# Optimization experiments

Measured on AMD Instinct MI355X. Metric: run time of the kernel, lower is better.

Reference implementation:

```python
import jax, jax.numpy as jnp
from jax import lax
import numpy as np

STATE_DIM = 64
CHANNELS = 128
SEQ_LEN = 4096
BATCH = 16
DT_MIN, DT_MAX = 1e-3, 1e-1


def hippo(n):
    # HiPPO-LegS construction, matching the torch staticmethod
    ar = jnp.arange(n, dtype=jnp.float32)
    P = jnp.sqrt(1.0 + 2.0 * ar)
    A = P[:, None] * P[None, :]
    A = jnp.tril(A) - jnp.diag(ar)
    B = jnp.sqrt(2.0 * ar + 1.0)
    return -A, B[:, None]


def setup_inputs() -> dict:
    key = jax.random.key(0)
    k_u, k_c = jax.random.split(key)
    A, B = hippo(STATE_DIM)
    # xavier_normal_ for C: std = sqrt(2/(fan_in+fan_out))
    std = float(np.sqrt(2.0 / (CHANNELS + STATE_DIM)))
    C = jax.random.normal(k_c, (CHANNELS, STATE_DIM), dtype=jnp.float32) * std
    D = jnp.ones((CHANNELS, 1), dtype=jnp.float32)
    # deterministic dt at log-midpoint of [dt_min, dt_max]
    dt = jnp.exp(jnp.array([(np.log(DT_MIN) + np.log(DT_MAX)) / 2.0], dtype=jnp.float32))
    u = jax.random.normal(k_u, (BATCH, SEQ_LEN), dtype=jnp.float32)
    return {"u": u, "A": A, "B": B, "C": C, "D": D, "dt": dt}


def reference(u, A, B, C, D, dt):
    # Training-path forward of LinearStateSpaceLayer (conv-kernel construction + conv1d)
    b, L = u.shape
    n = A.shape[0]
    dt_s = dt[0]
    I = jnp.eye(n, dtype=A.dtype)
    BL = jnp.linalg.inv(I - 0.5 * dt_s * A)            # bilinear discretization
    A_bar = BL @ (I + 0.5 * dt_s * A)                  # (n, n)
    B_bar = (BL * dt_s) @ B                            # (n, 1)

    # kernel k[j] = C @ A_bar^j @ B_bar for j = 0..L-1, via a scan of matvecs
    def step(v, _):
        return A_bar @ v, v
    _, vs = lax.scan(step, B_bar[:, 0], None, length=L)  # (L, n), vs[j] = A_bar^j B_bar
    k_causal = vs @ C.T                                  # (L, channels)
    # torch ordering: k_conv[c, 0, i] = C A_bar^{L-1-i} B_bar = k_causal[L-1-i, c]
    k_conv = k_causal[::-1].T[:, None, :]                # (channels, 1, L)

    # torch F.conv1d is cross-correlation; lax conv_general_dilated matches
    y = lax.conv_general_dilated(
        u[:, None, :], k_conv,
        window_strides=(1,), padding=[(L - 1, L - 1)],
        dimension_numbers=("NCH", "OIH", "NCH"),
    )[:, :, :L]                                          # (b, channels, L)

    # skip term: (u.unsqueeze(-1) @ D.T).transpose(-1,-2) == u[b,t] * D[c,0]
    y = y + u[:, None, :] * D[None, :, :]                # (b, channels, L)
    return y
```

## Files before the change

### kernel.cpp

```cpp
#include <hip/hip_runtime.h>

#define NS   64
#define CH   128
#define LSEQ 4096
#define NB   16
#define SCH  64
#define MCH  64
#define ST   68
#define CP   128

#define WS_ABAR 0
#define WS_A16  4096
#define WS_VS   8192
#define WS_BBAR 12288

#define X0_IDX(b, m) (((size_t)(b) * CH) * LSEQ + (size_t)(m) * SCH)

#define P_VSS  0
#define P_XCW  1024
#define P_XBS  1280
#define P_PLE  1536
#define P_PART 1792
#define P_A16  2048

#define FMA44(av, bv)                                                          \
    a0.x += av.x * bv.x; a0.y += av.x * bv.y; a0.z += av.x * bv.z; a0.w += av.x * bv.w; \
    a1.x += av.y * bv.x; a1.y += av.y * bv.y; a1.z += av.y * bv.z; a1.w += av.y * bv.w; \
    a2.x += av.z * bv.x; a2.y += av.z * bv.y; a2.z += av.z * bv.z; a2.w += av.z * bv.w; \
    a3.x += av.w * bv.x; a3.y += av.w * bv.y; a3.z += av.w * bv.z; a3.w += av.w * bv.w;


template<bool WT>
__device__ __forceinline__ void mm_square(const float* __restrict__ cm,
                                          const float* __restrict__ cmt,
                                          float* __restrict__ nm,
                                          float* __restrict__ nmt, int e) {
    const int l = e & 63;
    const int si0 = 16 * ((e >> 6) & 3) + 4 * (l >> 4);
    const int sj0 = 4 * (l & 15);
    const int kmax = si0 + 4;
    float4 a0 = {0,0,0,0}, a1 = {0,0,0,0}, a2 = {0,0,0,0}, a3 = {0,0,0,0};
    for (int k = 0; k < kmax; k += 4) {
        float4 av0 = *(const float4*)&cmt[(k + 0) * ST + si0];
        float4 bv0 = *(const float4*)&cm [(k + 0) * ST + sj0];
        float4 av1 = *(const float4*)&cmt[(k + 1) * ST + si0];
        float4 bv1 = *(const float4*)&cm [(k + 1) * ST + sj0];
        float4 av2 = *(const float4*)&cmt[(k + 2) * ST + si0];
        float4 bv2 = *(const float4*)&cm [(k + 2) * ST + sj0];
        float4 av3 = *(const float4*)&cmt[(k + 3) * ST + si0];
        float4 bv3 = *(const float4*)&cm [(k + 3) * ST + sj0];
        FMA44(av0, bv0)
        FMA44(av1, bv1)
        FMA44(av2, bv2)
        FMA44(av3, bv3)
    }
    *(float4*)&nm[(si0 + 0) * ST + sj0] = a0;
    *(float4*)&nm[(si0 + 1) * ST + sj0] = a1;
    *(float4*)&nm[(si0 + 2) * ST + sj0] = a2;
    *(float4*)&nm[(si0 + 3) * ST + sj0] = a3;
    if (WT) {
        float4 t0 = {a0.x, a1.x, a2.x, a3.x};
        float4 t1 = {a0.y, a1.y, a2.y, a3.y};
        float4 t2 = {a0.z, a1.z, a2.z, a3.z};
        float4 t3 = {a0.w, a1.w, a2.w, a3.w};
        *(float4*)&nmt[(sj0 + 0) * ST + si0] = t0;
        *(float4*)&nmt[(sj0 + 1) * ST + si0] = t1;
        *(float4*)&nmt[(sj0 + 2) * ST + si0] = t2;
        *(float4*)&nmt[(sj0 + 3) * ST + si0] = t3;
    }
}

__device__ __forceinline__ void mm_sq42(const float* __restrict__ cm,
                                        const float* __restrict__ cmt,
                                        float* __restrict__ nm,
                                        float* __restrict__ nmt, int tid) {
    const int si0 = 4 * (tid >> 5);
    const int sj0 = 2 * (tid & 31);
    const int kmax = si0 + 4;
    float2 a0 = {0,0}, a1 = {0,0}, a2 = {0,0}, a3 = {0,0};
#pragma unroll 4
    for (int k = 0; k < kmax; ++k) {
        float4 av = *(const float4*)&cmt[k * ST + si0];
        float2 bv = *(const float2*)&cm [k * ST + sj0];
        a0.x += av.x * bv.x; a0.y += av.x * bv.y;
        a1.x += av.y * bv.x; a1.y += av.y * bv.y;
        a2.x += av.z * bv.x; a2.y += av.z * bv.y;
        a3.x += av.w * bv.x; a3.y += av.w * bv.y;
    }
    *(float2*)&nm[(si0 + 0) * ST + sj0] = a0;
    *(float2*)&nm[(si0 + 1) * ST + sj0] = a1;
    *(float2*)&nm[(si0 + 2) * ST + sj0] = a2;
    *(float2*)&nm[(si0 + 3) * ST + sj0] = a3;
    float4 t0 = {a0.x, a1.x, a2.x, a3.x};
    float4 t1 = {a0.y, a1.y, a2.y, a3.y};
    *(float4*)&nmt[(sj0 + 0) * ST + si0] = t0;
    *(float4*)&nmt[(sj0 + 1) * ST + si0] = t1;
}

__device__ __forceinline__ void vs_expand1(const float* __restrict__ cmt,
                                           float* __restrict__ VT,
                                           int iq, int j, int mexp) {
    const int i0 = 4 * iq;
    float4 acc = {0,0,0,0};
#pragma unroll 8
    for (int k = 0; k < NS; ++k) {
        float4 av = *(const float4*)&cmt[k * ST + i0];
        float bk = VT[k * ST + j];
        acc.x += av.x * bk; acc.y += av.y * bk;
        acc.z += av.z * bk; acc.w += av.w * bk;
    }
    VT[(i0 + 0) * ST + mexp + j] = acc.x;
    VT[(i0 + 1) * ST + mexp + j] = acc.y;
    VT[(i0 + 2) * ST + mexp + j] = acc.z;
    VT[(i0 + 3) * ST + mexp + j] = acc.w;
}

__device__ __forceinline__ void pq_step(const float* __restrict__ Acol,
                                        const float* __restrict__ xle,
                                        float* __restrict__ outb, int r0, int e) {
    const int g = e >> 4, i0 = 4 * (e & 15);
    const float* bp = &xle[(4 * g + r0) * NS];
    float4 acc = *(const float4*)&xle[(4 * g + r0 + 1) * NS + i0];
#pragma unroll 8
    for (int k = 0; k < NS; ++k) {
        float4 av = *(const float4*)&Acol[k * ST + i0];
        float bk = bp[k];
        acc.x = fmaf(av.x, bk, acc.x); acc.y = fmaf(av.y, bk, acc.y);
        acc.z = fmaf(av.z, bk, acc.z); acc.w = fmaf(av.w, bk, acc.w);
    }
    *(float4*)&outb[g * ST + i0] = acc;
}

__device__ __forceinline__ void y_step512(const float* __restrict__ A128col,
                                          const float* __restrict__ P,
                                          const float* __restrict__ Q,
                                          float* __restrict__ Y, int e) {
    const int g = e >> 5, c0 = 2 * (e & 31);
    const float* bp = &P[g * ST];
    float2 acc = *(const float2*)&Q[g * ST + c0];
#pragma unroll 8
    for (int k = 0; k < NS; ++k) {
        float2 av = *(const float2*)&A128col[k * ST + c0];
        float bk = bp[k];
        acc.x = fmaf(av.x, bk, acc.x); acc.y = fmaf(av.y, bk, acc.y);
    }
    *(float2*)&Y[g * ST + c0] = acc;
}

__device__ __forceinline__ void inner_step(const float* __restrict__ Acol,
                                           const float* __restrict__ xle,
                                           float* __restrict__ stash, int r, int e) {
    const int g = e >> 4, i0 = 4 * (e & 15);
    const int mp = 4 * g + r - 1;
    float4 acc = *(const float4*)&xle[mp * NS + i0];
    const float* xp = &stash[mp * ST];
#pragma unroll 8
    for (int k = 0; k < NS; ++k) {
        float4 av = *(const float4*)&Acol[k * ST + i0];
        float xk = xp[k];
        acc.x = fmaf(av.x, xk, acc.x); acc.y = fmaf(av.y, xk, acc.y);
        acc.z = fmaf(av.z, xk, acc.z); acc.w = fmaf(av.w, xk, acc.w);
    }
    *(float4*)&stash[(mp + 1) * ST + i0] = acc;
}

__device__ __forceinline__ void inner512(const float* __restrict__ Acol,
                                         const float* __restrict__ xle,
                                         float* __restrict__ stash, int r, int e) {
    const int g = e >> 5, c0 = 2 * (e & 31);
    const int mp = 4 * g + r - 1;
    float2 acc = *(const float2*)&xle[mp * NS + c0];
    const float* xp = &stash[mp * ST];
#pragma unroll 8
    for (int k = 0; k < NS; ++k) {
        float2 av = *(const float2*)&Acol[k * ST + c0];
        float xk = xp[k];
        acc.x = fmaf(av.x, xk, acc.x); acc.y = fmaf(av.y, xk, acc.y);
    }
    *(float2*)&stash[(mp + 1) * ST + c0] = acc;
}

__device__ __forceinline__ void e1u_step(const float* __restrict__ A128col,
                                         const float* __restrict__ P,
                                         float* __restrict__ stash, int e) {
    const int g = e >> 4, i0 = 4 * (e & 15);
    const float* xp = &stash[(4 * g) * ST];
    float4 acc = *(const float4*)&P[g * ST + i0];
#pragma unroll 8
    for (int k = 0; k < NS; ++k) {
        float4 av = *(const float4*)&A128col[k * ST + i0];
        float xk = xp[k];
        acc.x = fmaf(av.x, xk, acc.x); acc.y = fmaf(av.y, xk, acc.y);
        acc.z = fmaf(av.z, xk, acc.z); acc.w = fmaf(av.w, xk, acc.w);
    }
    *(float4*)&stash[(4 * g + 2) * ST + i0] = acc;
}

__global__ __launch_bounds__(512) void k_sb(const float* __restrict__ u,
                                            const float* __restrict__ A,
                                            const float* __restrict__ Bv,
                                            const float* __restrict__ dtp,
                                            float* __restrict__ ws,
                                            float* __restrict__ out) {
    __shared__ __align__(16) float Mrow[NS * ST];
    __shared__ __align__(16) float Mcol[(NS + 1) * ST];
    __shared__ __align__(16) float Nrow[NS * ST];
    __shared__ __align__(16) float Ncol[NS * ST];
    __shared__ __align__(16) float VT[NS * ST];
    __shared__ __align__(16) float uT[NS * ST];
    __shared__ __align__(16) float vsS[NS * NS];
    __shared__ __align__(16) float xleS[MCH * NS];
    __shared__ __align__(16) float bcol[NS];
    __shared__ float rdiag[NS], xcS[NS];
    float* const stash = uT;
    float* const HbP = vsS;
    float* const HbQ = vsS + 16 * ST;
    float* const HbY = vsS + 32 * ST;
    const int tid = threadIdx.x;
    const int b = blockIdx.x;
    const float dt = dtp[0];
    const float hdt = 0.5f * dt;

    for (int o = tid; o < NS * NS; o += 512) {
        int i = o >> 6, k = o & 63;
        float a = A[o];
        float d = (i == k) ? 1.0f : 0.0f;
        Nrow[i * ST + k] = d - hdt * a;
        Ncol[k * ST + i] = d + hdt * a;
    }
    if (tid < NS) {
        bcol[tid]  = dt * Bv[tid];
        rdiag[tid] = 1.0f / (1.0f - hdt * A[tid * NS + tid]);
    }
    __syncthreads();

    {
        const int jj = tid & 63;
#pragma unroll
        for (int rep = 0; rep < 2; ++rep) {
            const int m0 = 4 * (tid >> 6) + 32 * rep;
            float4 v;
            v.x = u[b * LSEQ + (m0 + 0) * SCH + 63 - jj];
            v.y = u[b * LSEQ + (m0 + 1) * SCH + 63 - jj];
            v.z = u[b * LSEQ + (m0 + 2) * SCH + 63 - jj];
            v.w = u[b * LSEQ + (m0 + 3) * SCH + 63 - jj];
            *(float4*)&uT[jj * ST + m0] = v;
        }
    }

    if (tid <= NS) {
        float xr[NS];
        const float* t2b = (tid < NS) ? &Ncol[tid * ST] : bcol;
#pragma unroll
        for (int I = 0; I < 16; ++I) {
            const int i0 = 4 * I;
            float4 t2 = *(const float4*)&t2b[i0];
            float a0 = t2.x, a1 = t2.y, a2 = t2.z, a3 = t2.w;
#pragma unroll
            for (int k = 0; k < i0; k += 4) {
                float4 n0 = *(const float4*)&Nrow[(i0 + 0) * ST + k];
                float4 n1 = *(const float4*)&Nrow[(i0 + 1) * ST + k];
                float4 n2 = *(const float4*)&Nrow[(i0 + 2) * ST + k];
                float4 n3 = *(const float4*)&Nrow[(i0 + 3) * ST + k];
                a0 -= n0.x * xr[k] + n0.y * xr[k + 1] + n0.z * xr[k + 2] + n0.w * xr[k + 3];
                a1 -= n1.x * xr[k] + n1.y * xr[k + 1] + n1.z * xr[k + 2] + n1.w * xr[k + 3];
                a2 -= n2.x * xr[k] + n2.y * xr[k + 1] + n2.z * xr[k + 2] + n2.w * xr[k + 3];
                a3 -= n3.x * xr[k] + n3.y * xr[k + 1] + n3.z * xr[k + 2] + n3.w * xr[k + 3];
            }
            float4 rd  = *(const float4*)&rdiag[i0];
            float4 nb1 = *(const float4*)&Nrow[(i0 + 1) * ST + i0];
            float4 nb2 = *(const float4*)&Nrow[(i0 + 2) * ST + i0];
            float4 nb3 = *(const float4*)&Nrow[(i0 + 3) * ST + i0];
            float x0 = a0 * rd.x;
            float x1 = (a1 - nb1.x * x0) * rd.y;
            float x2 = (a2 - nb2.x * x0 - nb2.y * x1) * rd.z;
            float x3 = (a3 - nb3.x * x0 - nb3.y * x1 - nb3.z * x2) * rd.w;
            xr[i0 + 0] = x0; xr[i0 + 1] = x1; xr[i0 + 2] = x2; xr[i0 + 3] = x3;
        }
        float* xrow = &Mcol[tid * ST];
#pragma unroll
        for (int k = 0; k < NS; k += 4) {
            float4 v = {xr[k], xr[k + 1], xr[k + 2], xr[k + 3]};
            *(float4*)&xrow[k] = v;
        }
    }
    __syncthreads();

    if (tid < 256) {
        const int i0 = 4 * (tid >> 4), j0 = 4 * (tid & 15);
        float4 r0 = *(const float4*)&Mcol[(j0 + 0) * ST + i0];
        float4 r1 = *(const float4*)&Mcol[(j0 + 1) * ST + i0];
        float4 r2 = *(const float4*)&Mcol[(j0 + 2) * ST + i0];
        float4 r3 = *(const float4*)&Mcol[(j0 + 3) * ST + i0];
        float4 w0 = {r0.x, r1.x, r2.x, r3.x};
        float4 w1 = {r0.y, r1.y, r2.y, r3.y};
        float4 w2 = {r0.z, r1.z, r2.z, r3.z};
        float4 w3 = {r0.w, r1.w, r2.w, r3.w};
        *(float4*)&Mrow[(i0 + 0) * ST + j0] = w0;
        *(float4*)&Mrow[(i0 + 1) * ST + j0] = w1;
        *(float4*)&Mrow[(i0 + 2) * ST + j0] = w2;
        *(float4*)&Mrow[(i0 + 3) * ST + j0] = w3;
        if (b == 0) {
            *(float4*)&ws[WS_ABAR + (i0 + 0) * NS + j0] = w0;
            *(float4*)&ws[WS_ABAR + (i0 + 1) * NS + j0] = w1;
            *(float4*)&ws[WS_ABAR + (i0 + 2) * NS + j0] = w2;
            *(float4*)&ws[WS_ABAR + (i0 + 3) * NS + j0] = w3;
        }
    }
    if (b == 1 && tid < 16)
        *(float4*)&ws[WS_BBAR + 4 * tid] = *(const float4*)&Mcol[NS * ST + 4 * tid];
    if (tid < NS) VT[tid * ST + 0] = Mcol[NS * ST + tid];
    __syncthreads();

    float *cm = Mrow, *cmt = Mcol, *nm = Nrow, *nmt = Ncol;
    for (int s = 1; s <= 6; ++s) {
        if (s <= 4) {
            mm_sq42(cm, cmt, nm, nmt, tid);
            const int mexp = 1 << (s - 1);
            if (tid < 16 * mexp) {
                vs_expand1(cmt, VT, tid & 15, tid >> 4, mexp);
            }
        } else if (tid < 256) {
            mm_square<true>(cm, cmt, nm, nmt, tid);
        } else {
            const int e = tid - 256;
            const int iq = e & 15;
            if (s == 5) {
                vs_expand1(cmt, VT, iq, e >> 4, 16);
            } else {
                const int j0 = 2 * (e >> 4);
                const int i0 = 4 * iq;
                float4 c0 = {0,0,0,0}, c1 = {0,0,0,0};
#pragma unroll 8
                for (int k = 0; k < NS; ++k) {
                    float4 av = *(const float4*)&cmt[k * ST + i0];
                    float2 bv = *(const float2*)&VT[k * ST + j0];
                    c0.x += av.x * bv.x; c0.y += av.y * bv.x;
                    c0.z += av.z * bv.x; c0.w += av.w * bv.x;
                    c1.x += av.x * bv.y; c1.y += av.y * bv.y;
                    c1.z += av.z * bv.y; c1.w += av.w * bv.y;
                }
                float2 w0 = {c0.x, c1.x}, w1 = {c0.y, c1.y};
                float2 w2 = {c0.z, c1.z}, w3 = {c0.w, c1.w};
                *(float2*)&VT[(i0 + 0) * ST + 32 + j0] = w0;
                *(float2*)&VT[(i0 + 1) * ST + 32 + j0] = w1;
                *(float2*)&VT[(i0 + 2) * ST + 32 + j0] = w2;
                *(float2*)&VT[(i0 + 3) * ST + 32 + j0] = w3;
            }
        }
        __syncthreads();
        { float* t = cm; cm = nm; nm = t; t = cmt; cmt = nmt; nmt = t; }
        if (s == 4 && b == 2) {
            for (int o = tid; o < (NS * NS) / 4; o += 512) {
                int r = o >> 4, c4 = (o & 15) * 4;
                *(float4*)&ws[WS_A16 + r * NS + c4] = *(const float4*)&cm[r * ST + c4];
            }
        }
    }

    if (tid < 256) {
        const int i0 = 4 * (tid >> 4), j0 = 4 * (tid & 15);
        float4 v0 = *(const float4*)&VT[(i0 + 0) * ST + j0];
        float4 v1 = *(const float4*)&VT[(i0 + 1) * ST + j0];
        float4 v2 = *(const float4*)&VT[(i0 + 2) * ST + j0];
        float4 v3 = *(const float4*)&VT[(i0 + 3) * ST + j0];
        float4 w0 = {v0.x, v1.x, v2.x, v3.x};
        float4 w1 = {v0.y, v1.y, v2.y, v3.y};
        float4 w2 = {v0.z, v1.z, v2.z, v3.z};
        float4 w3 = {v0.w, v1.w, v2.w, v3.w};
        *(float4*)&vsS[(j0 + 0) * NS + i0] = w0;
        *(float4*)&vsS[(j0 + 1) * NS + i0] = w1;
        *(float4*)&vsS[(j0 + 2) * NS + i0] = w2;
        *(float4*)&vsS[(j0 + 3) * NS + i0] = w3;
        if (b == 3) {
            *(float4*)&ws[WS_VS + (j0 + 0) * NS + i0] = w0;
            *(float4*)&ws[WS_VS + (j0 + 1) * NS + i0] = w1;
            *(float4*)&ws[WS_VS + (j0 + 2) * NS + i0] = w2;
            *(float4*)&ws[WS_VS + (j0 + 3) * NS + i0] = w3;
        }
    } else {
        mm_square<true>(Mrow, Mcol, Nrow, Ncol, tid - 256);
    }
    __syncthreads();

    if (tid < 256) {
        const int ig = tid & 15, mg = tid >> 4;
        float4 a0 = {0,0,0,0}, a1 = {0,0,0,0}, a2 = {0,0,0,0}, a3 = {0,0,0,0};
#pragma unroll 4
        for (int j = 0; j < NS; j += 2) {
            float4 am  = *(const float4*)&uT[j * ST + 4 * mg];
            float4 bi  = *(const float4*)&vsS[j * NS + 4 * ig];
            float4 am2 = *(const float4*)&uT[(j + 1) * ST + 4 * mg];
            float4 bi2 = *(const float4*)&vsS[(j + 1) * NS + 4 * ig];
            FMA44(am, bi)
            FMA44(am2, bi2)
        }
        *(float4*)&xleS[(4 * mg + 0) * NS + 4 * ig] = a0;
        *(float4*)&xleS[(4 * mg + 1) * NS + 4 * ig] = a1;
        *(float4*)&xleS[(4 * mg + 2) * NS + 4 * ig] = a2;
        *(float4*)&xleS[(4 * mg + 3) * NS + 4 * ig] = a3;
    } else {
        mm_square<false>(Nrow, Ncol, VT, VT, tid - 256);
    }
    __syncthreads();

    if (tid < 256) pq_step(Mcol, xleS, HbP, 0, tid);
    else           pq_step(Mcol, xleS, HbQ, 2, tid - 256);
    if (tid < 64) { xcS[tid] = 0.f; stash[tid] = 0.f; }
    __syncthreads();

    y_step512(Ncol, HbP, HbQ, HbY, tid);
    __syncthreads();

    if (tid < 64) {
        const int i = tid;
        float4 arow[16];
#pragma unroll
        for (int c = 0; c < 16; ++c)
            arow[c] = *(const float4*)&VT[i * ST + 4 * c];
        float yv[15];
#pragma unroll
        for (int g = 0; g < 15; ++g) yv[g] = HbY[g * ST + i];
        for (int g = 0; g < 15; ++g) {
            float a0 = 0.f, a1 = 0.f, a2 = 0.f, a3 = 0.f;
#pragma unroll
            for (int c = 0; c < 16; ++c) {
                float4 xv = *(const float4*)&xcS[4 * c];
                a0 = fmaf(arow[c].x, xv.x, a0);
                a1 = fmaf(arow[c].y, xv.y, a1);
                a2 = fmaf(arow[c].z, xv.z, a2);
                a3 = fmaf(arow[c].w, xv.w, a3);
            }
            const float xn = ((a0 + a1) + (a2 + a3)) + yv[g];
            xcS[i] = xn;
            stash[(4 * g + 4) * ST + i] = xn;
        }
    }
    __syncthreads();

    if (tid < 256) inner_step(Mcol, xleS, stash, 1, tid);
    else           e1u_step(Ncol, HbP, stash, tid - 256);
    __syncthreads();

    inner512(Mcol, xleS, stash, 3, tid);
    __syncthreads();

    {
        const int m = tid >> 3, t8 = (tid & 7) * 8;
        float4 o1 = *(const float4*)&stash[m * ST + t8];
        float4 o2 = *(const float4*)&stash[m * ST + t8 + 4];
        *(float4*)&out[X0_IDX(b, m) + t8]     = o1;
        *(float4*)&out[X0_IDX(b, m) + t8 + 4] = o2;
    }
}

__global__ __launch_bounds__(256) void k_main2(const float* __restrict__ u,
                                               const float* __restrict__ Cm,
                                               const float* __restrict__ Dv,
                                               const float* __restrict__ ws,
                                               float* __restrict__ out) {
    __shared__ __align__(16) float Xl [NS * ST];
    __shared__ __align__(16) float Xl2[NS * ST];
    __shared__ __align__(16) float pool[NS * CP];
    __shared__ float uS[2][SCH], DS[CH], bbS[NS];
    const int mq = blockIdx.x, b = blockIdx.y;
    const int m0 = 2 * mq;
    const int tid = threadIdx.x;
    const int l = tid & 63, w = tid >> 6;

    for (int o = tid; o < (NS * NS) / 4; o += 256) {
        int r = o >> 4, c4 = (o & 15) * 4;
        *(float4*)&Xl[r * ST + c4]           = *(const float4*)&ws[WS_ABAR + r * NS + c4];
        *(float4*)&pool[P_A16 + r * NS + c4] = *(const float4*)&ws[WS_A16 + r * NS + c4];
    }
    for (int o = tid; o < 16 * NS; o += 256) pool[P_VSS + o] = ws[WS_VS + o];
    if (tid < NS) {
        uS[0][tid] = u[b * LSEQ + (m0 + 0) * SCH + tid];
        uS[1][tid] = u[b * LSEQ + (m0 + 1) * SCH + tid];
        bbS[tid]   = ws[WS_BBAR + tid];
    }
    if (tid < CH) DS[tid] = Dv[tid];
    __syncthreads();

    float4 arow[16];
#pragma unroll
    for (int c = 0; c < 16; ++c)
        arow[c] = *(const float4*)&Xl[l * ST + 4 * c];
    const float bbl = bbS[l];
    float4 a16r[4];
#pragma unroll
    for (int kq = 0; kq < 4; ++kq)
        a16r[kq] = *(const float4*)&pool[P_A16 + l * NS + 16 * w + 4 * kq];

    for (int c = 0; c < 2; ++c) {
        const int m = m0 + c;
        float* const Xp = c ? Xl2 : Xl;

        {
            float s = 0.f;
#pragma unroll
            for (int j = 0; j < 16; ++j) s += pool[P_VSS + j * NS + l] * uS[c][16 * w + 15 - j];
            pool[P_PLE + w * NS + l] = s;
        }
        if (tid < NS) pool[P_XBS + tid] = out[X0_IDX(b, m) + tid];
        __syncthreads();

        for (int p = 1; p < 4; ++p) {
            float4 x0q = *(const float4*)&pool[P_XBS + (p - 1) * NS + 16 * w + 0];
            float4 x1q = *(const float4*)&pool[P_XBS + (p - 1) * NS + 16 * w + 4];
            float4 x2q = *(const float4*)&pool[P_XBS + (p - 1) * NS + 16 * w + 8];
            float4 x3q = *(const float4*)&pool[P_XBS + (p - 1) * NS + 16 * w + 12];
            float s = a16r[0].x * x0q.x + a16r[0].y * x0q.y + a16r[0].z * x0q.z + a16r[0].w * x0q.w
                    + a16r[1].x * x1q.x + a16r[1].y * x1q.y + a16r[1].z * x1q.z + a16r[1].w * x1q.w
                    + a16r[2].x * x2q.x + a16r[2].y * x2q.y + a16r[2].z * x2q.z + a16r[2].w * x2q.w
                    + a16r[3].x * x3q.x + a16r[3].y * x3q.y + a16r[3].z * x3q.z + a16r[3].w * x3q.w;
            pool[P_PART + w * NS + l] = s;
            __syncthreads();
            if (w == 0) {
                float xn = pool[P_PART + l] + pool[P_PART + NS + l] + pool[P_PART + 2 * NS + l]
                         + pool[P_PART + 3 * NS + l] + pool[P_PLE + (p - 1) * NS + l];
                pool[P_XBS + p * NS + l] = xn;
            }
            __syncthreads();
        }

        float ur[16];
#pragma unroll
        for (int s = 0; s < 16; ++s) ur[s] = uS[c][16 * w + s];
        pool[P_XCW + w * NS + l] = pool[P_XBS + w * NS + l];
        for (int s = 0; s < 16; ++s) {
            const int t = 16 * w + s;
            float a0 = 0.f, a1 = 0.f, a2 = 0.f, a3 = 0.f;
#pragma unroll
            for (int cc = 0; cc < 16; ++cc) {
                float4 xv = *(const float4*)&pool[P_XCW + w * NS + 4 * cc];
                a0 = fmaf(arow[cc].x, xv.x, a0);
                a1 = fmaf(arow[cc].y, xv.y, a1);
                a2 = fmaf(arow[cc].z, xv.z, a2);
                a3 = fmaf(arow[cc].w, xv.w, a3);
            }
            const float xn = ((a0 + a1) + (a2 + a3)) + bbl * ur[s];
            pool[P_XCW + w * NS + l] = xn;
            Xp[l * ST + t] = xn;
        }
        __syncthreads();
    }

#pragma unroll
    for (int rep = 0; rep < 8; ++rep) {
        const int ii = tid & 63;
        const int cg = (tid >> 6) + 4 * rep;
        float4 v;
        v.x = Cm[(4 * cg + 0) * NS + ii];
        v.y = Cm[(4 * cg + 1) * NS + ii];
        v.z = Cm[(4 * cg + 2) * NS + ii];
        v.w = Cm[(4 * cg + 3) * NS + ii];
        *(float4*)&pool[ii * CP + 4 * cg] = v;
    }
    __syncthreads();

    for (int c = 0; c < 2; ++c) {
        const float* const Xp = c ? Xl2 : Xl;
        const int tg = tid & 7, cq = tid >> 3;
        float acc[4][8];
#pragma unroll
        for (int r = 0; r < 4; ++r)
#pragma unroll
            for (int cc = 0; cc < 8; ++cc) acc[r][cc] = 0.f;
#pragma unroll 4
        for (int ii = 0; ii < NS; ++ii) {
            float4 cv = *(const float4*)&pool[ii * CP + 4 * cq];
            float4 xa = *(const float4*)&Xp[ii * ST + 8 * tg + 0];
            float4 xb = *(const float4*)&Xp[ii * ST + 8 * tg + 4];
            float cr[4] = {cv.x, cv.y, cv.z, cv.w};
            float xv[8] = {xa.x, xa.y, xa.z, xa.w, xb.x, xb.y, xb.z, xb.w};
#pragma unroll
            for (int r = 0; r < 4; ++r)
#pragma unroll
                for (int cc = 0; cc < 8; ++cc) acc[r][cc] += cr[r] * xv[cc];
        }
        const size_t obase = ((size_t)b * CH) * LSEQ + (size_t)(m0 + c) * SCH + 8 * tg;
#pragma unroll
        for (int r = 0; r < 4; ++r) {
            const int ch = 4 * cq + r;
            const float dv = DS[ch];
            float4 o1, o2;
            o1.x = acc[r][0] + dv * uS[c][8 * tg + 0];
            o1.y = acc[r][1] + dv * uS[c][8 * tg + 1];
            o1.z = acc[r][2] + dv * uS[c][8 * tg + 2];
            o1.w = acc[r][3] + dv * uS[c][8 * tg + 3];
            o2.x = acc[r][4] + dv * uS[c][8 * tg + 4];
            o2.y = acc[r][5] + dv * uS[c][8 * tg + 5];
            o2.z = acc[r][6] + dv * uS[c][8 * tg + 6];
            o2.w = acc[r][7] + dv * uS[c][8 * tg + 7];
            float* op = out + obase + (size_t)ch * LSEQ;
            *(float4*)(op)     = o1;
            *(float4*)(op + 4) = o2;
        }
    }
}

extern "C" void kernel_launch(void* const* d_in, const int* in_sizes, int n_in,
                              void* d_out, int out_size, void* d_ws, size_t ws_size,
                              hipStream_t stream) {
    const float* u   = (const float*)d_in[0];
    const float* A   = (const float*)d_in[1];
    const float* Bv  = (const float*)d_in[2];
    const float* Cm  = (const float*)d_in[3];
    const float* Dv  = (const float*)d_in[4];
    const float* dtp = (const float*)d_in[5];
    float* ws  = (float*)d_ws;
    float* out = (float*)d_out;

    k_sb<<<NB, 512, 0, stream>>>(u, A, Bv, dtp, ws, out);
    k_main2<<<dim3(MCH / 2, NB), 256, 0, stream>>>(u, Cm, Dv, ws, out);
}
```

Before: 145.8 us.

## Process both sequence chunks concurrently in k_main2 with 512-thread blocks

k_main2 previously ran two chunks one after the other with 256 threads. It now launches 512 threads, and each 256-thread half handles one chunk, with its own scratch region in shared memory and its own output tile. The goal is to halve the serial recurrence and synchronisation chain per block by running both chunk recurrences in parallel. The cost is a larger block, which means more register pressure per block, and barriers that now cover both halves.

```diff
diff --git a/kernel.cpp b/kernel.cpp
--- a/kernel.cpp
+++ b/kernel.cpp
@@ -17,11 +17,11 @@
 #define X0_IDX(b, m) (((size_t)(b) * CH) * LSEQ + (size_t)(m) * SCH)
 
 #define P_VSS  0
-#define P_XCW  1024
-#define P_XBS  1280
-#define P_PLE  1536
-#define P_PART 1792
 #define P_A16  2048
+#define S_XCW  0
+#define S_XBS  256
+#define S_PLE  512
+#define S_PART 768
 
 #define FMA44(av, bv)                                                          \
     a0.x += av.x * bv.x; a0.y += av.x * bv.y; a0.z += av.x * bv.z; a0.w += av.x * bv.w; \
@@ -454,7 +454,7 @@
     }
 }
 
-__global__ __launch_bounds__(256) void k_main2(const float* __restrict__ u,
+__global__ __launch_bounds__(512) void k_main2(const float* __restrict__ u,
                                                const float* __restrict__ Cm,
                                                const float* __restrict__ Dv,
                                                const float* __restrict__ ws,
@@ -466,90 +466,90 @@
     const int mq = blockIdx.x, b = blockIdx.y;
     const int m0 = 2 * mq;
     const int tid = threadIdx.x;
-    const int l = tid & 63, w = tid >> 6;
-
-    for (int o = tid; o < (NS * NS) / 4; o += 256) {
+    const int c   = tid >> 8;
+    const int t8  = tid & 255;
+    const int l = t8 & 63, w = t8 >> 6;
+    const int SCR = c ? 6144 : 1024;
+    float* const Xp = c ? Xl2 : Xl;
+
+    for (int o = tid; o < (NS * NS) / 4; o += 512) {
         int r = o >> 4, c4 = (o & 15) * 4;
         *(float4*)&Xl[r * ST + c4]           = *(const float4*)&ws[WS_ABAR + r * NS + c4];
         *(float4*)&pool[P_A16 + r * NS + c4] = *(const float4*)&ws[WS_A16 + r * NS + c4];
     }
-    for (int o = tid; o < 16 * NS; o += 256) pool[P_VSS + o] = ws[WS_VS + o];
+    for (int o = tid; o < 16 * NS; o += 512) pool[P_VSS + o] = ws[WS_VS + o];
     if (tid < NS) {
         uS[0][tid] = u[b * LSEQ + (m0 + 0) * SCH + tid];
         uS[1][tid] = u[b * LSEQ + (m0 + 1) * SCH + tid];
         bbS[tid]   = ws[WS_BBAR + tid];
     }
     if (tid < CH) DS[tid] = Dv[tid];
+    if (t8 < NS) pool[SCR + S_XBS + t8] = out[X0_IDX(b, m0 + c) + t8];
     __syncthreads();
 
     float4 arow[16];
 #pragma unroll
-    for (int c = 0; c < 16; ++c)
-        arow[c] = *(const float4*)&Xl[l * ST + 4 * c];
+    for (int cc = 0; cc < 16; ++cc)
+        arow[cc] = *(const float4*)&Xl[l * ST + 4 * cc];
     const float bbl = bbS[l];
     float4 a16r[4];
 #pragma unroll
     for (int kq = 0; kq < 4; ++kq)
         a16r[kq] = *(const float4*)&pool[P_A16 + l * NS + 16 * w + 4 * kq];
-
-    for (int c = 0; c < 2; ++c) {
-        const int m = m0 + c;
-        float* const Xp = c ? Xl2 : Xl;
-
-        {
-            float s = 0.f;
-#pragma unroll
-            for (int j = 0; j < 16; ++j) s += pool[P_VSS + j * NS + l] * uS[c][16 * w + 15 - j];
-            pool[P_PLE + w * NS + l] = s;
-        }
-        if (tid < NS) pool[P_XBS + tid] = out[X0_IDX(b, m) + tid];
+    float ur[16];
+#pragma unroll
+    for (int s = 0; s < 16; ++s) ur[s] = uS[c][16 * w + s];
+
+    {
+        float s = 0.f;
+#pragma unroll
+        for (int j = 0; j < 16; ++j) s += pool[P_VSS + j * NS + l] * uS[c][16 * w + 15 - j];
+        pool[SCR + S_PLE + w * NS + l] = s;
+    }
+    __syncthreads();
+
+    for (int p = 1; p < 4; ++p) {
+        float4 x0q = *(const float4*)&pool[SCR + S_XBS + (p - 1) * NS + 16 * w + 0];
+        float4 x1q = *(const float4*)&pool[SCR + S_XBS + (p - 1) * NS + 16 * w + 4];
+        float4 x2q = *(const float4*)&pool[SCR + S_XBS + (p - 1) * NS + 16 * w + 8];
+        float4 x3q = *(const float4*)&pool[SCR + S_XBS + (p - 1) * NS + 16 * w + 12];
+        float s = a16r[0].x * x0q.x + a16r[0].y * x0q.y + a16r[0].z * x0q.z + a16r[0].w * x0q.w
+                + a16r[1].x * x1q.x + a16r[1].y * x1q.y + a16r[1].z * x1q.z + a16r[1].w * x1q.w
+                + a16r[2].x * x2q.x + a16r[2].y * x2q.y + a16r[2].z * x2q.z + a16r[2].w * x2q.w
+                + a16r[3].x * x3q.x + a16r[3].y * x3q.y + a16r[3].z * x3q.z + a16r[3].w * x3q.w;
+        pool[SCR + S_PART + w * NS + l] = s;
         __syncthreads();
-
-        for (int p = 1; p < 4; ++p) {
-            float4 x0q = *(const float4*)&pool[P_XBS + (p - 1) * NS + 16 * w + 0];
-            float4 x1q = *(const float4*)&pool[P_XBS + (p - 1) * NS + 16 * w + 4];
-            float4 x2q = *(const float4*)&pool[P_XBS + (p - 1) * NS + 16 * w + 8];
-            float4 x3q = *(const float4*)&pool[P_XBS + (p - 1) * NS + 16 * w + 12];
-            float s = a16r[0].x * x0q.x + a16r[0].y * x0q.y + a16r[0].z * x0q.z + a16r[0].w * x0q.w
-                    + a16r[1].x * x1q.x + a16r[1].y * x1q.y + a16r[1].z * x1q.z + a16r[1].w * x1q.w
-                    + a16r[2].x * x2q.x + a16r[2].y * x2q.y + a16r[2].z * x2q.z + a16r[2].w * x2q.w
-                    + a16r[3].x * x3q.x + a16r[3].y * x3q.y + a16r[3].z * x3q.z + a16r[3].w * x3q.w;
-            pool[P_PART + w * NS + l] = s;
-            __syncthreads();
-            if (w == 0) {
-                float xn = pool[P_PART + l] + pool[P_PART + NS + l] + pool[P_PART + 2 * NS + l]
-                         + pool[P_PART + 3 * NS + l] + pool[P_PLE + (p - 1) * NS + l];
-                pool[P_XBS + p * NS + l] = xn;
-            }
-            __syncthreads();
-        }
-
-        float ur[16];
-#pragma unroll
-        for (int s = 0; s < 16; ++s) ur[s] = uS[c][16 * w + s];
-        pool[P_XCW + w * NS + l] = pool[P_XBS + w * NS + l];
-        for (int s = 0; s < 16; ++s) {
-            const int t = 16 * w + s;
-            float a0 = 0.f, a1 = 0.f, a2 = 0.f, a3 = 0.f;
-#pragma unroll
-            for (int cc = 0; cc < 16; ++cc) {
-                float4 xv = *(const float4*)&pool[P_XCW + w * NS + 4 * cc];
-                a0 = fmaf(arow[cc].x, xv.x, a0);
-                a1 = fmaf(arow[cc].y, xv.y, a1);
-                a2 = fmaf(arow[cc].z, xv.z, a2);
-                a3 = fmaf(arow[cc].w, xv.w, a3);
-            }
-            const float xn = ((a0 + a1) + (a2 + a3)) + bbl * ur[s];
-            pool[P_XCW + w * NS + l] = xn;
-            Xp[l * ST + t] = xn;
+        if (w == 0) {
+            float xn = pool[SCR + S_PART + l] + pool[SCR + S_PART + NS + l]
+                     + pool[SCR + S_PART + 2 * NS + l] + pool[SCR + S_PART + 3 * NS + l]
+                     + pool[SCR + S_PLE + (p - 1) * NS + l];
+            pool[SCR + S_XBS + p * NS + l] = xn;
         }
         __syncthreads();
     }
 
-#pragma unroll
-    for (int rep = 0; rep < 8; ++rep) {
+    pool[SCR + S_XCW + w * NS + l] = pool[SCR + S_XBS + w * NS + l];
+    for (int s = 0; s < 16; ++s) {
+        const int t = 16 * w + s;
+        float a0 = 0.f, a1 = 0.f, a2 = 0.f, a3 = 0.f;
+#pragma unroll
+        for (int cc = 0; cc < 16; ++cc) {
+            float4 xv = *(const float4*)&pool[SCR + S_XCW + w * NS + 4 * cc];
+            a0 = fmaf(arow[cc].x, xv.x, a0);
+            a1 = fmaf(arow[cc].y, xv.y, a1);
+            a2 = fmaf(arow[cc].z, xv.z, a2);
+            a3 = fmaf(arow[cc].w, xv.w, a3);
+        }
+        const float xn = ((a0 + a1) + (a2 + a3)) + bbl * ur[s];
+        pool[SCR + S_XCW + w * NS + l] = xn;
+        Xp[l * ST + t] = xn;
+    }
+    __syncthreads();
+
+#pragma unroll
+    for (int rep = 0; rep < 4; ++rep) {
         const int ii = tid & 63;
-        const int cg = (tid >> 6) + 4 * rep;
+        const int cg = (tid >> 6) + 8 * rep;
         float4 v;
         v.x = Cm[(4 * cg + 0) * NS + ii];
         v.y = Cm[(4 * cg + 1) * NS + ii];
@@ -559,9 +559,8 @@
     }
     __syncthreads();
 
-    for (int c = 0; c < 2; ++c) {
-        const float* const Xp = c ? Xl2 : Xl;
-        const int tg = tid & 7, cq = tid >> 3;
+    {
+        const int tg = t8 & 7, cq = t8 >> 3;
         float acc[4][8];
 #pragma unroll
         for (int r = 0; r < 4; ++r)
@@ -613,5 +612,5 @@
     float* out = (float*)d_out;
 
     k_sb<<<NB, 512, 0, stream>>>(u, A, Bv, dtp, ws, out);
-    k_main2<<<dim3(MCH / 2, NB), 256, 0, stream>>>(u, Cm, Dv, ws, out);
-}
+    k_main2<<<dim3(MCH / 2, NB), 512, 0, stream>>>(u, Cm, Dv, ws, out);
+}
```

New measurement: 148.5 us. About the same (+1.9%).
